# Kernel optimization log

Hardware: AMD Instinct MI355X
Metric: run time of the kernel (lower is better)

## Reference

```python
import jax, jax.numpy as jnp
import numpy as np

B, T, D, F, E, K, L, S = 8, 1024, 512, 1024, 8, 2, 2, 64
SE, SH = 64, 128  # subject_embed_dim, style_hidden_dim


def setup_inputs() -> dict:
    key = jax.random.key(0)
    ks = jax.random.split(key, 16)
    r = lambda i, shape, s=0.05: (jax.random.normal(ks[i], shape, jnp.float32) * s)
    return dict(
        x=jax.random.normal(ks[0], (B, T, D), jnp.float32),
        subject_ids=jax.random.randint(ks[1], (B,), 0, S),
        # per-layer LayerNorm params (L, D)
        ln_g=jnp.ones((L, D), jnp.float32), ln_b=jnp.zeros((L, D), jnp.float32),
        # per-layer SubjectStyleAlignment params (weights stored (in, out))
        subj_emb=r(2, (L, S, SE), 0.02),
        h1_w=r(3, (L, SE, SH)), h1_b=jnp.zeros((L, SH), jnp.float32),
        h2_w=r(4, (L, SH, SH)), h2_b=jnp.zeros((L, SH), jnp.float32),
        s1_w=r(5, (L, SH, SH // 2)), s1_b=jnp.zeros((L, SH // 2), jnp.float32),
        s2_w=r(6, (L, SH // 2, 2 * D)), s2_b=jnp.zeros((L, 2 * D), jnp.float32),
        # shared TopKRouter: Linear(D, D//2) -> ReLU -> Linear(D//2, E)
        g1_w=r(7, (D, D // 2)), g1_b=jnp.zeros((D // 2,), jnp.float32),
        g2_w=r(8, (D // 2, E)), g2_b=jnp.zeros((E,), jnp.float32),
        # shared ExpertPool of GLU experts (no bias)
        wi0=r(9, (E, D, F)), wi1=r(10, (E, D, F)), wo=r(11, (E, F, D)),
    )


def _layernorm(x, g, b):
    m = x.mean(-1, keepdims=True)
    v = x.var(-1, keepdims=True)  # biased, matches torch LayerNorm
    return (x - m) / jnp.sqrt(v + 1e-5) * g + b


def reference(x, subject_ids, ln_g, ln_b, subj_emb, h1_w, h1_b, h2_w, h2_b,
              s1_w, s1_b, s2_w, s2_b, g1_w, g1_b, g2_w, g2_b, wi0, wi1, wo):
    Bs, Ts, Ds = x.shape
    for l in range(L):  # small fixed layer loop; expert pool + router are shared
        res = x
        h = _layernorm(x, ln_g[l], ln_b[l])
        # SubjectStyleAlignment: instance norm over time axis per (B, D) channel
        mu = h.mean(1, keepdims=True)
        var = h.var(1, keepdims=True)
        hn = (h - mu) / jnp.sqrt(var + 1e-8)
        e = subj_emb[l][subject_ids]                               # (B, SE)
        hh = jax.nn.relu(e @ h1_w[l] + h1_b[l]) @ h2_w[l] + h2_b[l]
        sp = jax.nn.relu(hh @ s1_w[l] + s1_b[l]) @ s2_w[l] + s2_b[l]  # (B, 2D)
        gamma = jax.nn.softplus(sp[:, :Ds]) + 1e-8
        beta = sp[:, Ds:]
        h = hn * gamma[:, None, :] + beta[:, None, :]
        # Router (shared across layers)
        hf = h.reshape(-1, Ds)                                     # (N, D)
        logits = jax.nn.relu(hf @ g1_w + g1_b) @ g2_w + g2_b       # (N, E)
        probs = jax.nn.softmax(logits, -1)
        gates, idx = jax.lax.top_k(probs, K)                       # (N, K)
        gates = gates / (gates.sum(-1, keepdims=True) + 1e-8)
        # combine weights: cw[n, e] = sum_k gates[n,k] * [idx[n,k]==e]
        cw = (jax.nn.one_hot(idx, E, dtype=hf.dtype) * gates[..., None]).sum(1)  # (N, E)
        # GLU experts, computed dense over E then gated-combined
        hid = jax.nn.relu(jnp.einsum('nd,edf->enf', hf, wi0)) \
              * jnp.einsum('nd,edf->enf', hf, wi1)                 # (E, N, F)
        eo = jnp.einsum('enf,efd->end', hid, wo)                   # (E, N, D)
        y = jnp.einsum('ne,end->nd', cw, eo)                       # (N, D)
        x = res + y.reshape(Bs, Ts, Ds)
    return x
```

## Files before the change

### kernel.cpp

```cpp
#include <hip/hip_runtime.h>

typedef unsigned short u16;
typedef unsigned int   u32;
typedef _Float16       f16;
typedef __attribute__((ext_vector_type(8))) _Float16 f16x8;
typedef __attribute__((ext_vector_type(4))) float    f32x4;
typedef __attribute__((ext_vector_type(4))) double   dbl4;

#define NSLOT_ 16384

__device__ __forceinline__ u16 f16bits(f16 h){ union{f16 f; u16 u;} x; x.f = h; return x.u; }

__device__ __forceinline__ void gl_lds16(const void* gptr, void* lptr){
  __builtin_amdgcn_global_load_lds((const __attribute__((address_space(1))) u32*)gptr,
                                   (__attribute__((address_space(3))) u32*)lptr, 16, 0, 0);
}

__device__ __forceinline__ int roff(int row, int lks){
  return ((row >> 1) << 6) + ((lks ^ ((row >> 1) & 3)) << 4) + ((row & 1) << 3);
}

__global__ __launch_bounds__(256) void ln_kernel(const float* __restrict__ x,
    const float* __restrict__ g, const float* __restrict__ bb, float* __restrict__ h){
  int n = blockIdx.x, t = threadIdx.x;
  const float* xr = x + ((size_t)n << 9);
  float2 v = *(const float2*)&xr[t*2];
  double vx = v.x, vy = v.y;
  double s = vx + vy;
  double q = vx*vx + vy*vy;
  #pragma unroll
  for (int o = 32; o > 0; o >>= 1){ s += __shfl_down(s, o, 64); q += __shfl_down(q, o, 64); }
  __shared__ double ls[4], lq_[4];
  __shared__ double sm, sv;
  int wid = t >> 6, lane = t & 63;
  if (lane == 0){ ls[wid] = s; lq_[wid] = q; }
  __syncthreads();
  if (t == 0){
    double S = ls[0]+ls[1]+ls[2]+ls[3], Q = lq_[0]+lq_[1]+lq_[2]+lq_[3];
    double mean = S * (1.0/512.0);
    double var  = Q * (1.0/512.0) - mean*mean;
    sm = mean; sv = 1.0/sqrt(var + 1e-5);
  }
  __syncthreads();
  double mean = sm, inv = sv;
  int d = t*2;
  float2 o;
  o.x = (float)((vx - mean)*inv*(double)g[d]   + (double)bb[d]);
  o.y = (float)((vy - mean)*inv*(double)g[d+1] + (double)bb[d+1]);
  *(float2*)&h[((size_t)n<<9) + d] = o;
}

__global__ __launch_bounds__(256) void colstats(const float* __restrict__ h,
    double* __restrict__ cs, double* __restrict__ cq){
  int bid = blockIdx.x;
  int b = bid >> 3, ch = bid & 7;
  int t = threadIdx.x;
  int col = ch*64 + (t & 63);
  int tp = t >> 6;
  const float* base = h + ((size_t)b << 19);
  double s = 0.0, q = 0.0;
  for (int tt = tp; tt < 1024; tt += 4){
    double v = (double)base[((size_t)tt << 9) + col];
    s += v; q += v*v;
  }
  __shared__ double ls[4][64], lq[4][64];
  ls[tp][t & 63] = s; lq[tp][t & 63] = q;
  __syncthreads();
  if (tp == 0){
    double S = ls[0][t]+ls[1][t]+ls[2][t]+ls[3][t];
    double Q = lq[0][t]+lq[1][t]+lq[2][t]+lq[3][t];
    cs[(b<<9)+col] = S; cq[(b<<9)+col] = Q;
  }
}

__global__ __launch_bounds__(256) void subj_kernel(const int* __restrict__ sid,
    const float* __restrict__ semb,
    const float* __restrict__ h1w, const float* __restrict__ h1b,
    const float* __restrict__ h2w, const float* __restrict__ h2b,
    const float* __restrict__ s1w, const float* __restrict__ s1b,
    const float* __restrict__ s2w, const float* __restrict__ s2b,
    const double* __restrict__ cs, const double* __restrict__ cq,
    double* __restrict__ a64, double* __restrict__ c64, int l){
  __shared__ double ev[64], hid1[128], hh[128], sh[64], sp[1024];
  int t = threadIdx.x;
  int b = blockIdx.x;
  int s = sid[b];
  if (t < 64) ev[t] = (double)semb[l*4096 + s*64 + t];
  __syncthreads();
  if (t < 128){
    double acc = (double)h1b[l*128 + t];
    for (int i = 0; i < 64; ++i) acc += ev[i]*(double)h1w[l*8192 + i*128 + t];
    hid1[t] = acc > 0.0 ? acc : 0.0;
  }
  __syncthreads();
  if (t < 128){
    double acc = (double)h2b[l*128 + t];
    for (int i = 0; i < 128; ++i) acc += hid1[i]*(double)h2w[l*16384 + i*128 + t];
    hh[t] = acc;
  }
  __syncthreads();
  if (t < 64){
    double acc = (double)s1b[l*64 + t];
    for (int i = 0; i < 128; ++i) acc += hh[i]*(double)s1w[l*8192 + i*64 + t];
    sh[t] = acc > 0.0 ? acc : 0.0;
  }
  __syncthreads();
  for (int m = t; m < 1024; m += 256){
    double acc = (double)s2b[l*1024 + m];
    for (int j = 0; j < 64; ++j) acc += sh[j]*(double)s2w[l*65536 + j*1024 + m];
    sp[m] = acc;
  }
  __syncthreads();
  for (int d = t; d < 512; d += 256){
    double mu  = cs[(b<<9)+d] * (1.0/1024.0);
    double var = cq[(b<<9)+d] * (1.0/1024.0) - mu*mu;
    double inv = 1.0/sqrt(var + 1e-8);
    double spv = sp[d];
    double gamma = (spv > 30.0 ? spv : log1p(exp(spv))) + 1e-8;
    double beta  = sp[512 + d];
    double A = gamma * inv;
    a64[(b<<9)+d] = A;
    c64[(b<<9)+d] = beta - mu*A;
  }
}

__global__ __launch_bounds__(256) void hfcast(const float* __restrict__ h,
    const double* __restrict__ a64, const double* __restrict__ c64,
    u16* __restrict__ hfh, u16* __restrict__ hfl){
  size_t i0 = ((size_t)blockIdx.x*256 + threadIdx.x) * 8;
  int n = (int)(i0 >> 9);
  int d0 = (int)(i0 & 511);
  int b = n >> 10;
// ... 111 lines not shown
      double v = l0[e];
      if (v > b1){ b2 = b1; i2 = i1; b1 = v; i1 = e; }
      else if (v > b2){ b2 = v; i2 = e; }
    }
    double pr1 = p[i1]/s, pr2 = p[i2]/s;
    double den = pr1 + pr2 + 1e-8;
    int n = tok0 + t;
    idxo[2*n] = i1; idxo[2*n+1] = i2;
    wo_[2*n] = (float)(pr1/den); wo_[2*n+1] = (float)(pr2/den);
    atomicAdd(&lcnt[i1], 1); atomicAdd(&lcnt[i2], 1);
  }
  __syncthreads();
  if (t < 8) atomicAdd(&counts[t], lcnt[t]);
}

__global__ void offsets_kernel(const int* __restrict__ counts, int* __restrict__ offs,
                               int* __restrict__ cur){
  if (threadIdx.x == 0 && blockIdx.x == 0){
    int run = 0;
    for (int e = 0; e < 8; ++e){ offs[e] = run; run += counts[e]; cur[e] = 0; }
  }
}

__global__ __launch_bounds__(256) void scatter_kernel(const int* __restrict__ idx,
    const int* __restrict__ offs, int* __restrict__ cur,
    int* __restrict__ tok_of, int* __restrict__ slot_of){
  __shared__ int lcnt[8], lbase[8];
  int t = threadIdx.x;
  int n = blockIdx.x*256 + t;
  if (t < 8) lcnt[t] = 0;
  __syncthreads();
  int e0 = idx[2*n], e1 = idx[2*n+1];
  int p0 = atomicAdd(&lcnt[e0], 1);
  int p1 = atomicAdd(&lcnt[e1], 1);
  __syncthreads();
  if (t < 8) lbase[t] = atomicAdd(&cur[t], lcnt[t]);
  __syncthreads();
  int s0 = offs[e0] + lbase[e0] + p0;
  int s1 = offs[e1] + lbase[e1] + p1;
  tok_of[s0] = n; tok_of[s1] = n;
  slot_of[2*n] = s0; slot_of[2*n+1] = s1;
}

__global__ __launch_bounds__(256) void cvtT16(const float* __restrict__ src,
    u16* __restrict__ dh, u16* __restrict__ dl, int R, int C){
  int bx = blockIdx.x;
  int tilesC = C >> 5, tilesR = R >> 5;
  int e = bx / (tilesR*tilesC);
  int rem = bx % (tilesR*tilesC);
  int rt = rem / tilesC, ct = rem % tilesC;
  __shared__ float tile[32][33];
  int t = threadIdx.x;
  int j = t & 31, i0 = t >> 5;
  const float* s = src + (size_t)e*R*C + (size_t)(rt*32)*C + ct*32;
  for (int ii = i0; ii < 32; ii += 8) tile[ii][j] = s[(size_t)ii*C + j];
  __syncthreads();
  size_t ob = (size_t)e*R*C + (size_t)(ct*32)*R + rt*32;
  for (int ii = i0; ii < 32; ii += 8){
    float v = tile[j][ii];
    f16 hi = (f16)v;
    float rem2 = (v - (float)hi) * 2048.f;
    f16 lo = (f16)rem2;
    dh[ob + (size_t)ii*R + j] = f16bits(hi);
    dl[ob + (size_t)ii*R + j] = f16bits(lo);
  }
}

__global__ __launch_bounds__(256) void up1_kernel(const u16* __restrict__ hfh,
    const u16* __restrict__ hfl,
    const u16* __restrict__ w0h, const u16* __restrict__ w0l,
    const u16* __restrict__ w1h, const u16* __restrict__ w1l,
    const int* __restrict__ tok_of, const int* __restrict__ offs, const int* __restrict__ counts,
    u16* __restrict__ hidh, u16* __restrict__ hidl){
  int bx = blockIdx.x;
  int e  = bx >> 11;
  int mt = (bx >> 4) & 127;
  int nt = bx & 15;
  int base = offs[e], cnt = counts[e];
  int row0 = mt << 7;
  if (row0 >= cnt) return;
  __shared__ __align__(16) u16 Ah[2][4096], Alo[2][4096];
  __shared__ __align__(16) u16 B0h[2][2048], B0l[2][2048], B1h[2][2048], B1l[2][2048];
  int t = threadIdx.x, w = t >> 6, l = t & 63;
  int wm = w >> 1, wn = w & 1;
  int lr = l & 15, lks = l >> 4;
  int riw = ((l >> 3) << 1) | (l & 1);
  int kc16s = ((((l >> 1) & 3) ^ ((l >> 3) & 3)) << 3);
  int ar1 = w*16 + riw;
  int tokA1, tokA2;
  { int ss = base + row0 + ar1;      ss = ss < NSLOT_ ? ss : NSLOT_-1; tokA1 = tok_of[ss]; }
  { int ss = base + row0 + 64 + ar1; ss = ss < NSLOT_ ? ss : NSLOT_-1; tokA2 = tok_of[ss]; }
  const u16* sAh1 = hfh + ((size_t)tokA1 << 9) + kc16s;
  const u16* sAh2 = hfh + ((size_t)tokA2 << 9) + kc16s;
  const u16* sAl1 = hfl + ((size_t)tokA1 << 9) + kc16s;
  const u16* sAl2 = hfl + ((size_t)tokA2 << 9) + kc16s;
  size_t bcol = (size_t)(e*1024 + nt*64);
  size_t bci = (bcol + (size_t)ar1) << 9;
  const u16* sB0h = w0h + bci + kc16s;
  const u16* sB0l = w0l + bci + kc16s;
  const u16* sB1h = w1h + bci + kc16s;
  const u16* sB1l = w1l + bci + kc16s;
  int aoff[4], boff[2];
  #pragma unroll
  for (int mi = 0; mi < 4; ++mi) aoff[mi] = roff(wm*64 + mi*16 + lr, lks);
  #pragma unroll
  for (int ni = 0; ni < 2; ++ni) boff[ni] = roff(wn*32 + ni*16 + lr, lks);
  f32x4 hh0[4][2], cr0[4][2], hh1[4][2], cr1[4][2];
  #pragma unroll
  for (int i = 0; i < 4; ++i)
    #pragma unroll
    for (int j = 0; j < 2; ++j)
      #pragma unroll
      for (int r = 0; r < 4; ++r){ hh0[i][j][r]=0.f; cr0[i][j][r]=0.f; hh1[i][j][r]=0.f; cr1[i][j][r]=0.f; }
#define STG_U(buf, kc) do{ \
    gl_lds16(sAh1 + (kc), &Ah[buf][t*8]); \
    gl_lds16(sAh2 + (kc), &Ah[buf][2048 + t*8]); \
    gl_lds16(sAl1 + (kc), &Alo[buf][t*8]); \
    gl_lds16(sAl2 + (kc), &Alo[buf][2048 + t*8]); \
    gl_lds16(sB0h + (kc), &B0h[buf][t*8]); \
    gl_lds16(sB0l + (kc), &B0l[buf][t*8]); \
    gl_lds16(sB1h + (kc), &B1h[buf][t*8]); \
    gl_lds16(sB1l + (kc), &B1l[buf][t*8]); }while(0)
  STG_U(0, 0);
  for (int ks = 0; ks < 16; ++ks){
    int cur = ks & 1;
    __syncthreads();
    if (ks < 15) STG_U(cur^1, (ks+1)*32);
    f16x8 ah[4], al[4], b0hv[2], b0lv[2], b1hv[2], b1lv[2];
    #pragma unroll
    for (int mi = 0; mi < 4; ++mi){
      ah[mi] = *(const f16x8*)&Ah[cur][aoff[mi]];
      al[mi] = *(const f16x8*)&Alo[cur][aoff[mi]];
    }
    #pragma unroll
    for (int ni = 0; ni < 2; ++ni){
      b0hv[ni] = *(const f16x8*)&B0h[cur][boff[ni]];
      b0lv[ni] = *(const f16x8*)&B0l[cur][boff[ni]];
      b1hv[ni] = *(const f16x8*)&B1h[cur][boff[ni]];
      b1lv[ni] = *(const f16x8*)&B1l[cur][boff[ni]];
    }
    #pragma unroll
    for (int mi = 0; mi < 4; ++mi)
      #pragma unroll
      for (int ni = 0; ni < 2; ++ni){
        hh0[mi][ni] = __builtin_amdgcn_mfma_f32_16x16x32_f16(ah[mi], b0hv[ni], hh0[mi][ni], 0, 0, 0);
        hh1[mi][ni] = __builtin_amdgcn_mfma_f32_16x16x32_f16(ah[mi], b1hv[ni], hh1[mi][ni], 0, 0, 0);
        cr0[mi][ni] = __builtin_amdgcn_mfma_f32_16x16x32_f16(ah[mi], b0lv[ni], cr0[mi][ni], 0, 0, 0);
        cr0[mi][ni] = __builtin_amdgcn_mfma_f32_16x16x32_f16(al[mi], b0hv[ni], cr0[mi][ni], 0, 0, 0);
        cr1[mi][ni] = __builtin_amdgcn_mfma_f32_16x16x32_f16(ah[mi], b1lv[ni], cr1[mi][ni], 0, 0, 0);
        cr1[mi][ni] = __builtin_amdgcn_mfma_f32_16x16x32_f16(al[mi], b1hv[ni], cr1[mi][ni], 0, 0, 0);
      }
  }
#undef STG_U
  #pragma unroll
  for (int mi = 0; mi < 4; ++mi){
    int rb = row0 + wm*64 + mi*16 + lks*4;
    #pragma unroll
    for (int r = 0; r < 4; ++r){
      int rr = rb + r;
      if (rr < cnt){
        size_t orow = ((size_t)(base + rr) << 10) + nt*64;
        #pragma unroll
        for (int ni = 0; ni < 2; ++ni){
          int col = wn*32 + ni*16 + lr;
          float u0 = hh0[mi][ni][r] + cr0[mi][ni][r]*(1.f/2048.f);
          float u1 = hh1[mi][ni][r] + cr1[mi][ni][r]*(1.f/2048.f);
          u0 = u0 > 0.f ? u0 : 0.f;
          float v = u0*u1;
          f16 vh = (f16)v;
          float rem = (v - (float)vh)*2048.f;
          hidh[orow + col] = f16bits(vh);
          hidl[orow + col] = f16bits((f16)rem);
        }
      }
    }
  }
}

__global__ __launch_bounds__(256) void down1_kernel(const u16* __restrict__ hidh,
    const u16* __restrict__ hidl, const u16* __restrict__ wdh, const u16* __restrict__ wdl,
    const int* __restrict__ offs, const int* __restrict__ counts, float* __restrict__ eo){
  int bx = blockIdx.x;
  int e  = bx >> 10;
  int mt = (bx >> 3) & 127;
  int nt = bx & 7;
  int base = offs[e], cnt = counts[e];
  int row0 = mt << 7;
  if (row0 >= cnt) return;
  __shared__ __align__(16) u16 Ah[2][4096], Alo[2][4096];
  __shared__ __align__(16) u16 Bh[2][2048], Bl[2][2048];
  int t = threadIdx.x, w = t >> 6, l = t & 63;
  int wm = w >> 1, wn = w & 1;
  int lr = l & 15, lks = l >> 4;
  int riw = ((l >> 3) << 1) | (l & 1);
  int kc16s = ((((l >> 1) & 3) ^ ((l >> 3) & 3)) << 3);
  int ar1 = w*16 + riw;
  int sA1c = base + row0 + ar1;      sA1c = sA1c < NSLOT_ ? sA1c : NSLOT_-1;
  int sA2c = base + row0 + 64 + ar1; sA2c = sA2c < NSLOT_ ? sA2c : NSLOT_-1;
  const u16* sAh1 = hidh + ((size_t)sA1c << 10) + kc16s;
  const u16* sAh2 = hidh + ((size_t)sA2c << 10) + kc16s;
  const u16* sAl1 = hidl + ((size_t)sA1c << 10) + kc16s;
  const u16* sAl2 = hidl + ((size_t)sA2c << 10) + kc16s;
  size_t bcol = (size_t)(e*512 + nt*64);
  size_t bci = (bcol + (size_t)ar1) << 10;
  const u16* sBh = wdh + bci + kc16s;
  const u16* sBl = wdl + bci + kc16s;
  int aoff[4], boff[2];
  #pragma unroll
  for (int mi = 0; mi < 4; ++mi) aoff[mi] = roff(wm*64 + mi*16 + lr, lks);
  #pragma unroll
  for (int ni = 0; ni < 2; ++ni) boff[ni] = roff(wn*32 + ni*16 + lr, lks);
  f32x4 hh[4][2], cr[4][2];
  #pragma unroll
  for (int i = 0; i < 4; ++i)
    #pragma unroll
    for (int j = 0; j < 2; ++j)
      #pragma unroll
      for (int r = 0; r < 4; ++r){ hh[i][j][r]=0.f; cr[i][j][r]=0.f; }
#define STG_D(buf, kc) do{ \
    gl_lds16(sAh1 + (kc), &Ah[buf][t*8]); \
    gl_lds16(sAh2 + (kc), &Ah[buf][2048 + t*8]); \
    gl_lds16(sAl1 + (kc), &Alo[buf][t*8]); \
    gl_lds16(sAl2 + (kc), &Alo[buf][2048 + t*8]); \
    gl_lds16(sBh + (kc), &Bh[buf][t*8]); \
    gl_lds16(sBl + (kc), &Bl[buf][t*8]); }while(0)
  STG_D(0, 0);
  for (int ks = 0; ks < 32; ++ks){
    int cur = ks & 1;
    __syncthreads();
    if (ks < 31) STG_D(cur^1, (ks+1)*32);
    f16x8 ah[4], al[4], bh[2], bl[2];
    #pragma unroll
    for (int mi = 0; mi < 4; ++mi){
      ah[mi] = *(const f16x8*)&Ah[cur][aoff[mi]];
      al[mi] = *(const f16x8*)&Alo[cur][aoff[mi]];
    }
    #pragma unroll
    for (int ni = 0; ni < 2; ++ni){
      bh[ni] = *(const f16x8*)&Bh[cur][boff[ni]];
      bl[ni] = *(const f16x8*)&Bl[cur][boff[ni]];
    }
    #pragma unroll
    for (int mi = 0; mi < 4; ++mi)
      #pragma unroll
      for (int ni = 0; ni < 2; ++ni){
        hh[mi][ni] = __builtin_amdgcn_mfma_f32_16x16x32_f16(ah[mi], bh[ni], hh[mi][ni], 0, 0, 0);
        cr[mi][ni] = __builtin_amdgcn_mfma_f32_16x16x32_f16(ah[mi], bl[ni], cr[mi][ni], 0, 0, 0);
        cr[mi][ni] = __builtin_amdgcn_mfma_f32_16x16x32_f16(al[mi], bh[ni], cr[mi][ni], 0, 0, 0);
      }
  }
#undef STG_D
  #pragma unroll
  for (int mi = 0; mi < 4; ++mi){
    int rb = row0 + wm*64 + mi*16 + lks*4;
    #pragma unroll
    for (int r = 0; r < 4; ++r){
      int rr = rb + r;
      if (rr < cnt){
        float* orow = eo + (((size_t)(base + rr)) << 9) + nt*64;
        #pragma unroll
        for (int ni = 0; ni < 2; ++ni)
          orow[wn*32 + ni*16 + lr] = hh[mi][ni][r] + cr[mi][ni][r]*(1.f/2048.f);
      }
    }
  }
}

__global__ __launch_bounds__(256) void uph_kernel(const u16* __restrict__ hfh,
    const u16* __restrict__ w0h, const u16* __restrict__ w1h,
    const int* __restrict__ tok_of, const int* __restrict__ offs, const int* __restrict__ counts,
    u16* __restrict__ hidh){
  int bx = blockIdx.x;
  int e  = bx >> 11;
  int mt = (bx >> 4) & 127;
  int nt = bx & 15;
  int base = offs[e], cnt = counts[e];
  int row0 = mt << 7;
  if (row0 >= cnt) return;
  __shared__ __align__(16) u16 Ah[2][4096];
  __shared__ __align__(16) u16 B0h[2][2048], B1h[2][2048];
  int t = threadIdx.x, w = t >> 6, l = t & 63;
  int wm = w >> 1, wn = w & 1;
  int lr = l & 15, lks = l >> 4;
  int riw = ((l >> 3) << 1) | (l & 1);
  int kc16s = ((((l >> 1) & 3) ^ ((l >> 3) & 3)) << 3);
  int ar1 = w*16 + riw;
  int tokA1, tokA2;
  { int ss = base + row0 + ar1;      ss = ss < NSLOT_ ? ss : NSLOT_-1; tokA1 = tok_of[ss]; }
  { int ss = base + row0 + 64 + ar1; ss = ss < NSLOT_ ? ss : NSLOT_-1; tokA2 = tok_of[ss]; }
  const u16* sAh1 = hfh + ((size_t)tokA1 << 9) + kc16s;
  const u16* sAh2 = hfh + ((size_t)tokA2 << 9) + kc16s;
  size_t bcol = (size_t)(e*1024 + nt*64);
  size_t bci = (bcol + (size_t)ar1) << 9;
  const u16* sB0 = w0h + bci + kc16s;
  const u16* sB1 = w1h + bci + kc16s;
  int aoff[4], boff[2];
  #pragma unroll
  for (int mi = 0; mi < 4; ++mi) aoff[mi] = roff(wm*64 + mi*16 + lr, lks);
  #pragma unroll
  for (int ni = 0; ni < 2; ++ni) boff[ni] = roff(wn*32 + ni*16 + lr, lks);
  f32x4 hh0[4][2], hh1[4][2];
  #pragma unroll
  for (int i = 0; i < 4; ++i)
    #pragma unroll
    for (int j = 0; j < 2; ++j)
      #pragma unroll
      for (int r = 0; r < 4; ++r){ hh0[i][j][r]=0.f; hh1[i][j][r]=0.f; }
#define STG_UH(buf, kc) do{ \
    gl_lds16(sAh1 + (kc), &Ah[buf][t*8]); \
    gl_lds16(sAh2 + (kc), &Ah[buf][2048 + t*8]); \
    gl_lds16(sB0 + (kc), &B0h[buf][t*8]); \
    gl_lds16(sB1 + (kc), &B1h[buf][t*8]); }while(0)
  STG_UH(0, 0);
  for (int ks = 0; ks < 16; ++ks){
    int cur = ks & 1;
    __syncthreads();
    if (ks < 15) STG_UH(cur^1, (ks+1)*32);
    f16x8 ah[4], b0v[2], b1v[2];
    #pragma unroll
    for (int mi = 0; mi < 4; ++mi) ah[mi] = *(const f16x8*)&Ah[cur][aoff[mi]];
    #pragma unroll
    for (int ni = 0; ni < 2; ++ni){
      b0v[ni] = *(const f16x8*)&B0h[cur][boff[ni]];
      b1v[ni] = *(const f16x8*)&B1h[cur][boff[ni]];
    }
    #pragma unroll
    for (int mi = 0; mi < 4; ++mi)
      #pragma unroll
      for (int ni = 0; ni < 2; ++ni){
        hh0[mi][ni] = __builtin_amdgcn_mfma_f32_16x16x32_f16(ah[mi], b0v[ni], hh0[mi][ni], 0, 0, 0);
        hh1[mi][ni] = __builtin_amdgcn_mfma_f32_16x16x32_f16(ah[mi], b1v[ni], hh1[mi][ni], 0, 0, 0);
      }
  }
#undef STG_UH
  #pragma unroll
  for (int mi = 0; mi < 4; ++mi){
    int rb = row0 + wm*64 + mi*16 + lks*4;
    #pragma unroll
    for (int r = 0; r < 4; ++r){
      int rr = rb + r;
      if (rr < cnt){
        size_t orow = ((size_t)(base + rr) << 10) + nt*64;
        #pragma unroll
        for (int ni = 0; ni < 2; ++ni){
          int col = wn*32 + ni*16 + lr;
          float u0 = hh0[mi][ni][r];
          u0 = u0 > 0.f ? u0 : 0.f;
          hidh[orow + col] = f16bits((f16)(u0*hh1[mi][ni][r]));
        }
      }
    }
  }
}

__global__ __launch_bounds__(256) void dnh_kernel(const u16* __restrict__ hidh,
    const u16* __restrict__ wdh,
    const int* __restrict__ offs, const int* __restrict__ counts, float* __restrict__ eo){
  int bx = blockIdx.x;
  int e  = bx >> 10;
  int mt = (bx >> 3) & 127;
  int nt = bx & 7;
  int base = offs[e], cnt = counts[e];
  int row0 = mt << 7;
  if (row0 >= cnt) return;
  __shared__ __align__(16) u16 Ah[2][4096];
  __shared__ __align__(16) u16 Bh[2][2048];
  int t = threadIdx.x, w = t >> 6, l = t & 63;
  int wm = w >> 1, wn = w & 1;
  int lr = l & 15, lks = l >> 4;
  int riw = ((l >> 3) << 1) | (l & 1);
  int kc16s = ((((l >> 1) & 3) ^ ((l >> 3) & 3)) << 3);
  int ar1 = w*16 + riw;
  int sA1c = base + row0 + ar1;      sA1c = sA1c < NSLOT_ ? sA1c : NSLOT_-1;
  int sA2c = base + row0 + 64 + ar1; sA2c = sA2c < NSLOT_ ? sA2c : NSLOT_-1;
  const u16* sAh1 = hidh + ((size_t)sA1c << 10) + kc16s;
  const u16* sAh2 = hidh + ((size_t)sA2c << 10) + kc16s;
  size_t bcol = (size_t)(e*512 + nt*64);
  const u16* sB = wdh + ((bcol + (size_t)ar1) << 10) + kc16s;
  int aoff[4], boff[2];
  #pragma unroll
  for (int mi = 0; mi < 4; ++mi) aoff[mi] = roff(wm*64 + mi*16 + lr, lks);
  #pragma unroll
  for (int ni = 0; ni < 2; ++ni) boff[ni] = roff(wn*32 + ni*16 + lr, lks);
  f32x4 hh[4][2];
  #pragma unroll
  for (int i = 0; i < 4; ++i)
    #pragma unroll
    for (int j = 0; j < 2; ++j)
      #pragma unroll
      for (int r = 0; r < 4; ++r) hh[i][j][r] = 0.f;
#define STG_DH(buf, kc) do{ \
    gl_lds16(sAh1 + (kc), &Ah[buf][t*8]); \
    gl_lds16(sAh2 + (kc), &Ah[buf][2048 + t*8]); \
    gl_lds16(sB + (kc), &Bh[buf][t*8]); }while(0)
  STG_DH(0, 0);
  for (int ks = 0; ks < 32; ++ks){
    int cur = ks & 1;
    __syncthreads();
    if (ks < 31) STG_DH(cur^1, (ks+1)*32);
    f16x8 ah[4], bh[2];
    #pragma unroll
    for (int mi = 0; mi < 4; ++mi) ah[mi] = *(const f16x8*)&Ah[cur][aoff[mi]];
    #pragma unroll
    for (int ni = 0; ni < 2; ++ni) bh[ni] = *(const f16x8*)&Bh[cur][boff[ni]];
    #pragma unroll
    for (int mi = 0; mi < 4; ++mi)
      #pragma unroll
      for (int ni = 0; ni < 2; ++ni)
        hh[mi][ni] = __builtin_amdgcn_mfma_f32_16x16x32_f16(ah[mi], bh[ni], hh[mi][ni], 0, 0, 0);
  }
#undef STG_DH
  #pragma unroll
  for (int mi = 0; mi < 4; ++mi){
    int rb = row0 + wm*64 + mi*16 + lks*4;
    #pragma unroll
    for (int r = 0; r < 4; ++r){
      int rr = rb + r;
      if (rr < cnt){
        float* orow = eo + (((size_t)(base + rr)) << 9) + nt*64;
        #pragma unroll
        for (int ni = 0; ni < 2; ++ni)
          orow[wn*32 + ni*16 + lr] = hh[mi][ni][r];
      }
    }
  }
}

__global__ __launch_bounds__(128) void gather_kernel(const float* __restrict__ xin,
    const float* __restrict__ eo, const int* __restrict__ slot_of, const float* __restrict__ wv,
    float* __restrict__ out){
  int n = blockIdx.x, t = threadIdx.x;
  int s0 = slot_of[2*n], s1 = slot_of[2*n+1];
  double w0 = wv[2*n], w1 = wv[2*n+1];
  float4 xi = *(const float4*)&xin[((size_t)n << 9) + t*4];
  float4 e0 = *(const float4*)&eo[((size_t)s0 << 9) + t*4];
  float4 e1 = *(const float4*)&eo[((size_t)s1 << 9) + t*4];
  float4 o;
  o.x = (float)((double)xi.x + w0*(double)e0.x + w1*(double)e1.x);
  o.y = (float)((double)xi.y + w0*(double)e0.y + w1*(double)e1.y);
  o.z = (float)((double)xi.z + w0*(double)e0.z + w1*(double)e1.z);
  o.w = (float)((double)xi.w + w0*(double)e0.w + w1*(double)e1.w);
  *(float4*)&out[((size_t)n << 9) + t*4] = o;
}

extern "C" void kernel_launch(void* const* d_in, const int* in_sizes, int n_in,
                              void* d_out, int out_size, void* d_ws, size_t ws_size,
                              hipStream_t stream) {
  (void)in_sizes; (void)n_in; (void)out_size; (void)ws_size;
  const float* x0   = (const float*)d_in[0];
  const int*   sid  = (const int*)  d_in[1];
  const float* ln_g = (const float*)d_in[2];
  const float* ln_b = (const float*)d_in[3];
  const float* semb = (const float*)d_in[4];
  const float* h1w  = (const float*)d_in[5];
  const float* h1b  = (const float*)d_in[6];
  const float* h2w  = (const float*)d_in[7];
  const float* h2b  = (const float*)d_in[8];
  const float* s1w  = (const float*)d_in[9];
  const float* s1b  = (const float*)d_in[10];
  const float* s2w  = (const float*)d_in[11];
  const float* s2b  = (const float*)d_in[12];
  const float* g1w  = (const float*)d_in[13];
  const float* g1b  = (const float*)d_in[14];
  const float* g2w  = (const float*)d_in[15];
  const float* g2b  = (const float*)d_in[16];
  const float* wi0  = (const float*)d_in[17];
  const float* wi1  = (const float*)d_in[18];
  const float* wo   = (const float*)d_in[19];

  char* W = (char*)d_ws;
  float*  h      = (float*)(W + 0);
  u16*    hfh    = (u16*)  (W + 16777216ULL);
  u16*    hfl    = (u16*)  (W + 25165824ULL);
  float*  eo32   = (float*)(W + 0);
  u16*    hid16h = (u16*)  (W + 33554432ULL);
  u16*    hid16l = (u16*)  (W + 67108864ULL);
  u16*    w0Th   = (u16*)  (W + 100663296ULL);
  u16*    w0Tl   = (u16*)  (W + 109051904ULL);
  u16*    w1Th   = (u16*)  (W + 117440512ULL);
  u16*    w1Tl   = (u16*)  (W + 125829120ULL);
  u16*    woTh   = (u16*)  (W + 134217728ULL);
  u16*    woTl   = (u16*)  (W + 142606336ULL);
  u16*    g1Th   = (u16*)  (W + 150994944ULL);
  u16*    g1Tl   = (u16*)  (W + 151257088ULL);
  double* cs     = (double*)(W + 151519232ULL);
  double* cq     = (double*)(W + 151552000ULL);
  double* a64    = (double*)(W + 151584768ULL);
  double* c64    = (double*)(W + 151617536ULL);
  int*    idxa   = (int*)   (W + 151650304ULL);
  float*  warr   = (float*) (W + 151715840ULL);
  int*    tok_of = (int*)   (W + 151781376ULL);
  int*    slot_of= (int*)   (W + 151846912ULL);
  int*    counts = (int*)   (W + 151912448ULL);
  int*    cur    = counts + 8;
  int*    offs   = counts + 16;

  cvtT16<<<4096, 256, 0, stream>>>(wi0, w0Th, w0Tl, 512, 1024);
  cvtT16<<<4096, 256, 0, stream>>>(wi1, w1Th, w1Tl, 512, 1024);
  cvtT16<<<4096, 256, 0, stream>>>(wo,  woTh, woTl, 1024, 512);
  cvtT16<<<128,  256, 0, stream>>>(g1w, g1Th, g1Tl, 512, 256);

  for (int l = 0; l < 2; ++l){
    const float* xin = l ? (const float*)d_out : x0;
    ln_kernel<<<8192, 256, 0, stream>>>(xin, ln_g + l*512, ln_b + l*512, h);
    colstats<<<64, 256, 0, stream>>>(h, cs, cq);
    subj_kernel<<<8, 256, 0, stream>>>(sid, semb, h1w, h1b, h2w, h2b, s1w, s1b, s2w, s2b,
                                       cs, cq, a64, c64, l);
    hfcast<<<2048, 256, 0, stream>>>(h, a64, c64, hfh, hfl);
    zero_counts<<<1, 64, 0, stream>>>(counts);
    gate2_kernel<<<512, 256, 0, stream>>>(hfh, hfl, g1Th, g1Tl, g1b, g2w, g2b, idxa, warr, counts);
    offsets_kernel<<<1, 1, 0, stream>>>(counts, offs, cur);
    scatter_kernel<<<32, 256, 0, stream>>>(idxa, offs, cur, tok_of, slot_of);
    if (l == 0){
      up1_kernel<<<16384, 256, 0, stream>>>(hfh, hfl, w0Th, w0Tl, w1Th, w1Tl,
                                            tok_of, offs, counts, hid16h, hid16l);
      down1_kernel<<<8192, 256, 0, stream>>>(hid16h, hid16l, woTh, woTl, offs, counts, eo32);
    } else {
      uph_kernel<<<16384, 256, 0, stream>>>(hfh, w0Th, w1Th, tok_of, offs, counts, hid16h);
      dnh_kernel<<<8192, 256, 0, stream>>>(hid16h, woTh, offs, counts, eo32);
    }
    gather_kernel<<<8192, 128, 0, stream>>>(xin, eo32, slot_of, warr, (float*)d_out);
  }
}
```

Before: 868.7 us.

## Widen MoE GEMM N-tiles and fuse layer-0 gather with layer-1 LayerNorm

The down and up expert GEMM kernels (dnh, uph, down1) now use 128-column output tiles instead of 64, halving the grid and reusing each staged A tile across twice as many outputs. up1 keeps 64 columns but switches its warp layout from 2x2 to 4x1 over rows. The layer loop is unrolled, and a new gather_ln kernel fuses the layer-0 residual combine with the layer-1 LayerNorm, which removes one full pass over the activations. eo32 moves to its own workspace region so it no longer overlaps h. The wider tiles raise accumulator register and LDS use, which can lower occupancy.

```diff
diff --git a/kernel.cpp b/kernel.cpp
--- a/kernel.cpp
+++ b/kernel.cpp
@@ -48,6 +48,49 @@
   o.x = (float)((vx - mean)*inv*(double)g[d]   + (double)bb[d]);
   o.y = (float)((vy - mean)*inv*(double)g[d+1] + (double)bb[d+1]);
   *(float2*)&h[((size_t)n<<9) + d] = o;
+}
+
+__global__ __launch_bounds__(128) void gather_ln(const float* __restrict__ xin,
+    const float* __restrict__ eo, const int* __restrict__ slot_of, const float* __restrict__ wv,
+    const float* __restrict__ g, const float* __restrict__ bb,
+    float* __restrict__ out, float* __restrict__ h){
+  int n = blockIdx.x, t = threadIdx.x;
+  int s0 = slot_of[2*n], s1 = slot_of[2*n+1];
+  double w0 = wv[2*n], w1 = wv[2*n+1];
+  float4 xi = *(const float4*)&xin[((size_t)n << 9) + t*4];
+  float4 e0 = *(const float4*)&eo[((size_t)s0 << 9) + t*4];
+  float4 e1 = *(const float4*)&eo[((size_t)s1 << 9) + t*4];
+  double o0 = (double)xi.x + w0*(double)e0.x + w1*(double)e1.x;
+  double o1 = (double)xi.y + w0*(double)e0.y + w1*(double)e1.y;
+  double o2 = (double)xi.z + w0*(double)e0.z + w1*(double)e1.z;
+  double o3 = (double)xi.w + w0*(double)e0.w + w1*(double)e1.w;
+  float4 o; o.x = (float)o0; o.y = (float)o1; o.z = (float)o2; o.w = (float)o3;
+  *(float4*)&out[((size_t)n << 9) + t*4] = o;
+  double vx = o.x, vy = o.y, vz = o.z, vw = o.w;
+  double s = vx+vy+vz+vw;
+  double q = vx*vx+vy*vy+vz*vz+vw*vw;
+  #pragma unroll
+  for (int off = 32; off > 0; off >>= 1){ s += __shfl_down(s, off, 64); q += __shfl_down(q, off, 64); }
+  __shared__ double ls[2], lq_[2];
+  __shared__ double sm, sv;
+  int wid = t >> 6, lane = t & 63;
+  if (lane == 0){ ls[wid] = s; lq_[wid] = q; }
+  __syncthreads();
+  if (t == 0){
+    double S = ls[0]+ls[1], Q = lq_[0]+lq_[1];
+    double mean = S * (1.0/512.0);
+    double var  = Q * (1.0/512.0) - mean*mean;
+    sm = mean; sv = 1.0/sqrt(var + 1e-5);
+  }
+  __syncthreads();
+  double mean = sm, inv = sv;
+  int d = t*4;
+  float4 ho;
+  ho.x = (float)((vx - mean)*inv*(double)g[d]   + (double)bb[d]);
+  ho.y = (float)((vy - mean)*inv*(double)g[d+1] + (double)bb[d+1]);
+  ho.z = (float)((vz - mean)*inv*(double)g[d+2] + (double)bb[d+2]);
+  ho.w = (float)((vw - mean)*inv*(double)g[d+3] + (double)bb[d+3]);
+  *(float4*)&h[((size_t)n<<9) + d] = ho;
 }
 
 __global__ __launch_bounds__(256) void colstats(const float* __restrict__ h,
@@ -325,7 +368,6 @@
   __shared__ __align__(16) u16 Ah[2][4096], Alo[2][4096];
   __shared__ __align__(16) u16 B0h[2][2048], B0l[2][2048], B1h[2][2048], B1l[2][2048];
   int t = threadIdx.x, w = t >> 6, l = t & 63;
-  int wm = w >> 1, wn = w & 1;
   int lr = l & 15, lks = l >> 4;
   int riw = ((l >> 3) << 1) | (l & 1);
   int kc16s = ((((l >> 1) & 3) ^ ((l >> 3) & 3)) << 3);
@@ -343,16 +385,16 @@
   const u16* sB0l = w0l + bci + kc16s;
   const u16* sB1h = w1h + bci + kc16s;
   const u16* sB1l = w1l + bci + kc16s;
-  int aoff[4], boff[2];
-  #pragma unroll
-  for (int mi = 0; mi < 4; ++mi) aoff[mi] = roff(wm*64 + mi*16 + lr, lks);
-  #pragma unroll
-  for (int ni = 0; ni < 2; ++ni) boff[ni] = roff(wn*32 + ni*16 + lr, lks);
-  f32x4 hh0[4][2], cr0[4][2], hh1[4][2], cr1[4][2];
-  #pragma unroll
-  for (int i = 0; i < 4; ++i)
-    #pragma unroll
-    for (int j = 0; j < 2; ++j)
+  int aoff[2], boff[4];
+  #pragma unroll
+  for (int mi = 0; mi < 2; ++mi) aoff[mi] = roff(w*32 + mi*16 + lr, lks);
+  #pragma unroll
+  for (int ni = 0; ni < 4; ++ni) boff[ni] = roff(ni*16 + lr, lks);
+  f32x4 hh0[2][4], cr0[2][4], hh1[2][4], cr1[2][4];
+  #pragma unroll
+  for (int i = 0; i < 2; ++i)
+    #pragma unroll
+    for (int j = 0; j < 4; ++j)
       #pragma unroll
       for (int r = 0; r < 4; ++r){ hh0[i][j][r]=0.f; cr0[i][j][r]=0.f; hh1[i][j][r]=0.f; cr1[i][j][r]=0.f; }
 #define STG_U(buf, kc) do{ \
@@ -369,23 +411,23 @@
     int cur = ks & 1;
     __syncthreads();
     if (ks < 15) STG_U(cur^1, (ks+1)*32);
-    f16x8 ah[4], al[4], b0hv[2], b0lv[2], b1hv[2], b1lv[2];
-    #pragma unroll
-    for (int mi = 0; mi < 4; ++mi){
+    f16x8 ah[2], al[2], b0hv[4], b0lv[4], b1hv[4], b1lv[4];
+    #pragma unroll
+    for (int mi = 0; mi < 2; ++mi){
       ah[mi] = *(const f16x8*)&Ah[cur][aoff[mi]];
       al[mi] = *(const f16x8*)&Alo[cur][aoff[mi]];
     }
     #pragma unroll
-    for (int ni = 0; ni < 2; ++ni){
+    for (int ni = 0; ni < 4; ++ni){
       b0hv[ni] = *(const f16x8*)&B0h[cur][boff[ni]];
       b0lv[ni] = *(const f16x8*)&B0l[cur][boff[ni]];
       b1hv[ni] = *(const f16x8*)&B1h[cur][boff[ni]];
       b1lv[ni] = *(const f16x8*)&B1l[cur][boff[ni]];
     }
     #pragma unroll
-    for (int mi = 0; mi < 4; ++mi)
+    for (int mi = 0; mi < 2; ++mi)
       #pragma unroll
-      for (int ni = 0; ni < 2; ++ni){
+      for (int ni = 0; ni < 4; ++ni){
         hh0[mi][ni] = __builtin_amdgcn_mfma_f32_16x16x32_f16(ah[mi], b0hv[ni], hh0[mi][ni], 0, 0, 0);
         hh1[mi][ni] = __builtin_amdgcn_mfma_f32_16x16x32_f16(ah[mi], b1hv[ni], hh1[mi][ni], 0, 0, 0);
         cr0[mi][ni] = __builtin_amdgcn_mfma_f32_16x16x32_f16(ah[mi], b0lv[ni], cr0[mi][ni], 0, 0, 0);
@@ -396,16 +438,16 @@
   }
 #undef STG_U
   #pragma unroll
-  for (int mi = 0; mi < 4; ++mi){
-    int rb = row0 + wm*64 + mi*16 + lks*4;
+  for (int mi = 0; mi < 2; ++mi){
+    int rb = row0 + w*32 + mi*16 + lks*4;
     #pragma unroll
     for (int r = 0; r < 4; ++r){
       int rr = rb + r;
       if (rr < cnt){
         size_t orow = ((size_t)(base + rr) << 10) + nt*64;
         #pragma unroll
-        for (int ni = 0; ni < 2; ++ni){
-          int col = wn*32 + ni*16 + lr;
+        for (int ni = 0; ni < 4; ++ni){
+          int col = ni*16 + lr;
           float u0 = hh0[mi][ni][r] + cr0[mi][ni][r]*(1.f/2048.f);
           float u1 = hh1[mi][ni][r] + cr1[mi][ni][r]*(1.f/2048.f);
           u0 = u0 > 0.f ? u0 : 0.f;
@@ -424,14 +466,14 @@
     const u16* __restrict__ hidl, const u16* __restrict__ wdh, const u16* __restrict__ wdl,
     const int* __restrict__ offs, const int* __restrict__ counts, float* __restrict__ eo){
   int bx = blockIdx.x;
-  int e  = bx >> 10;
-  int mt = (bx >> 3) & 127;
-  int nt = bx & 7;
+  int e  = bx >> 9;
+  int mt = (bx >> 2) & 127;
+  int nt = bx & 3;
   int base = offs[e], cnt = counts[e];
   int row0 = mt << 7;
   if (row0 >= cnt) return;
   __shared__ __align__(16) u16 Ah[2][4096], Alo[2][4096];
-  __shared__ __align__(16) u16 Bh[2][2048], Bl[2][2048];
+  __shared__ __align__(16) u16 Bh[2][4096], Bl[2][4096];
   int t = threadIdx.x, w = t >> 6, l = t & 63;
   int wm = w >> 1, wn = w & 1;
   int lr = l & 15, lks = l >> 4;
@@ -444,20 +486,21 @@
   const u16* sAh2 = hidh + ((size_t)sA2c << 10) + kc16s;
   const u16* sAl1 = hidl + ((size_t)sA1c << 10) + kc16s;
   const u16* sAl2 = hidl + ((size_t)sA2c << 10) + kc16s;
-  size_t bcol = (size_t)(e*512 + nt*64);
-  size_t bci = (bcol + (size_t)ar1) << 10;
-  const u16* sBh = wdh + bci + kc16s;
-  const u16* sBl = wdl + bci + kc16s;
-  int aoff[4], boff[2];
+  size_t bcol = (size_t)(e*512 + nt*128);
+  const u16* sBh1 = wdh + ((bcol + (size_t)ar1) << 10) + kc16s;
+  const u16* sBh2 = wdh + ((bcol + 64 + (size_t)ar1) << 10) + kc16s;
+  const u16* sBl1 = wdl + ((bcol + (size_t)ar1) << 10) + kc16s;
+  const u16* sBl2 = wdl + ((bcol + 64 + (size_t)ar1) << 10) + kc16s;
+  int aoff[4], boff[4];
   #pragma unroll
   for (int mi = 0; mi < 4; ++mi) aoff[mi] = roff(wm*64 + mi*16 + lr, lks);
   #pragma unroll
-  for (int ni = 0; ni < 2; ++ni) boff[ni] = roff(wn*32 + ni*16 + lr, lks);
-  f32x4 hh[4][2], cr[4][2];
+  for (int ni = 0; ni < 4; ++ni) boff[ni] = roff(wn*64 + ni*16 + lr, lks);
+  f32x4 hh[4][4], cr[4][4];
   #pragma unroll
   for (int i = 0; i < 4; ++i)
     #pragma unroll
-    for (int j = 0; j < 2; ++j)
+    for (int j = 0; j < 4; ++j)
       #pragma unroll
       for (int r = 0; r < 4; ++r){ hh[i][j][r]=0.f; cr[i][j][r]=0.f; }
 #define STG_D(buf, kc) do{ \
@@ -465,28 +508,30 @@
     gl_lds16(sAh2 + (kc), &Ah[buf][2048 + t*8]); \
     gl_lds16(sAl1 + (kc), &Alo[buf][t*8]); \
     gl_lds16(sAl2 + (kc), &Alo[buf][2048 + t*8]); \
-    gl_lds16(sBh + (kc), &Bh[buf][t*8]); \
-    gl_lds16(sBl + (kc), &Bl[buf][t*8]); }while(0)
+    gl_lds16(sBh1 + (kc), &Bh[buf][t*8]); \
+    gl_lds16(sBh2 + (kc), &Bh[buf][2048 + t*8]); \
+    gl_lds16(sBl1 + (kc), &Bl[buf][t*8]); \
+    gl_lds16(sBl2 + (kc), &Bl[buf][2048 + t*8]); }while(0)
   STG_D(0, 0);
   for (int ks = 0; ks < 32; ++ks){
     int cur = ks & 1;
     __syncthreads();
     if (ks < 31) STG_D(cur^1, (ks+1)*32);
-    f16x8 ah[4], al[4], bh[2], bl[2];
+    f16x8 ah[4], al[4], bh[4], bl[4];
     #pragma unroll
     for (int mi = 0; mi < 4; ++mi){
       ah[mi] = *(const f16x8*)&Ah[cur][aoff[mi]];
       al[mi] = *(const f16x8*)&Alo[cur][aoff[mi]];
     }
     #pragma unroll
-    for (int ni = 0; ni < 2; ++ni){
+    for (int ni = 0; ni < 4; ++ni){
       bh[ni] = *(const f16x8*)&Bh[cur][boff[ni]];
       bl[ni] = *(const f16x8*)&Bl[cur][boff[ni]];
     }
     #pragma unroll
     for (int mi = 0; mi < 4; ++mi)
       #pragma unroll
-      for (int ni = 0; ni < 2; ++ni){
+      for (int ni = 0; ni < 4; ++ni){
         hh[mi][ni] = __builtin_amdgcn_mfma_f32_16x16x32_f16(ah[mi], bh[ni], hh[mi][ni], 0, 0, 0);
         cr[mi][ni] = __builtin_amdgcn_mfma_f32_16x16x32_f16(ah[mi], bl[ni], cr[mi][ni], 0, 0, 0);
         cr[mi][ni] = __builtin_amdgcn_mfma_f32_16x16x32_f16(al[mi], bh[ni], cr[mi][ni], 0, 0, 0);
@@ -500,10 +545,10 @@
     for (int r = 0; r < 4; ++r){
       int rr = rb + r;
       if (rr < cnt){
-        float* orow = eo + (((size_t)(base + rr)) << 9) + nt*64;
+        float* orow = eo + (((size_t)(base + rr)) << 9) + nt*128;
         #pragma unroll
-        for (int ni = 0; ni < 2; ++ni)
-          orow[wn*32 + ni*16 + lr] = hh[mi][ni][r] + cr[mi][ni][r]*(1.f/2048.f);
+        for (int ni = 0; ni < 4; ++ni)
+          orow[wn*64 + ni*16 + lr] = hh[mi][ni][r] + cr[mi][ni][r]*(1.f/2048.f);
       }
     }
   }
@@ -514,14 +559,14 @@
     const int* __restrict__ tok_of, const int* __restrict__ offs, const int* __restrict__ counts,
     u16* __restrict__ hidh){
   int bx = blockIdx.x;
-  int e  = bx >> 11;
-  int mt = (bx >> 4) & 127;
-  int nt = bx & 15;
+  int e  = bx >> 10;
+  int mt = (bx >> 3) & 127;
+  int nt = bx & 7;
   int base = offs[e], cnt = counts[e];
   int row0 = mt << 7;
   if (row0 >= cnt) return;
   __shared__ __align__(16) u16 Ah[2][4096];
-  __shared__ __align__(16) u16 B0h[2][2048], B1h[2][2048];
+  __shared__ __align__(16) u16 B0[2][4096], B1[2][4096];
   int t = threadIdx.x, w = t >> 6, l = t & 63;
   int wm = w >> 1, wn = w & 1;
   int lr = l & 15, lks = l >> 4;
@@ -533,44 +578,47 @@
   { int ss = base + row0 + 64 + ar1; ss = ss < NSLOT_ ? ss : NSLOT_-1; tokA2 = tok_of[ss]; }
   const u16* sAh1 = hfh + ((size_t)tokA1 << 9) + kc16s;
   const u16* sAh2 = hfh + ((size_t)tokA2 << 9) + kc16s;
-  size_t bcol = (size_t)(e*1024 + nt*64);
-  size_t bci = (bcol + (size_t)ar1) << 9;
-  const u16* sB0 = w0h + bci + kc16s;
-  const u16* sB1 = w1h + bci + kc16s;
-  int aoff[4], boff[2];
+  size_t bcol = (size_t)(e*1024 + nt*128);
+  const u16* sB0a = w0h + ((bcol + (size_t)ar1) << 9) + kc16s;
+  const u16* sB0b = w0h + ((bcol + 64 + (size_t)ar1) << 9) + kc16s;
+  const u16* sB1a = w1h + ((bcol + (size_t)ar1) << 9) + kc16s;
+  const u16* sB1b = w1h + ((bcol + 64 + (size_t)ar1) << 9) + kc16s;
+  int aoff[4], boff[4];
   #pragma unroll
   for (int mi = 0; mi < 4; ++mi) aoff[mi] = roff(wm*64 + mi*16 + lr, lks);
   #pragma unroll
-  for (int ni = 0; ni < 2; ++ni) boff[ni] = roff(wn*32 + ni*16 + lr, lks);
-  f32x4 hh0[4][2], hh1[4][2];
+  for (int ni = 0; ni < 4; ++ni) boff[ni] = roff(wn*64 + ni*16 + lr, lks);
+  f32x4 hh0[4][4], hh1[4][4];
   #pragma unroll
   for (int i = 0; i < 4; ++i)
     #pragma unroll
-    for (int j = 0; j < 2; ++j)
+    for (int j = 0; j < 4; ++j)
       #pragma unroll
       for (int r = 0; r < 4; ++r){ hh0[i][j][r]=0.f; hh1[i][j][r]=0.f; }
 #define STG_UH(buf, kc) do{ \
     gl_lds16(sAh1 + (kc), &Ah[buf][t*8]); \
     gl_lds16(sAh2 + (kc), &Ah[buf][2048 + t*8]); \
-    gl_lds16(sB0 + (kc), &B0h[buf][t*8]); \
-    gl_lds16(sB1 + (kc), &B1h[buf][t*8]); }while(0)
+    gl_lds16(sB0a + (kc), &B0[buf][t*8]); \
+    gl_lds16(sB0b + (kc), &B0[buf][2048 + t*8]); \
+    gl_lds16(sB1a + (kc), &B1[buf][t*8]); \
+    gl_lds16(sB1b + (kc), &B1[buf][2048 + t*8]); }while(0)
   STG_UH(0, 0);
   for (int ks = 0; ks < 16; ++ks){
     int cur = ks & 1;
     __syncthreads();
     if (ks < 15) STG_UH(cur^1, (ks+1)*32);
-    f16x8 ah[4], b0v[2], b1v[2];
+    f16x8 ah[4], b0v[4], b1v[4];
     #pragma unroll
     for (int mi = 0; mi < 4; ++mi) ah[mi] = *(const f16x8*)&Ah[cur][aoff[mi]];
     #pragma unroll
-    for (int ni = 0; ni < 2; ++ni){
-      b0v[ni] = *(const f16x8*)&B0h[cur][boff[ni]];
-      b1v[ni] = *(const f16x8*)&B1h[cur][boff[ni]];
+    for (int ni = 0; ni < 4; ++ni){
+      b0v[ni] = *(const f16x8*)&B0[cur][boff[ni]];
+      b1v[ni] = *(const f16x8*)&B1[cur][boff[ni]];
     }
     #pragma unroll
     for (int mi = 0; mi < 4; ++mi)
       #pragma unroll
-      for (int ni = 0; ni < 2; ++ni){
+      for (int ni = 0; ni < 4; ++ni){
         hh0[mi][ni] = __builtin_amdgcn_mfma_f32_16x16x32_f16(ah[mi], b0v[ni], hh0[mi][ni], 0, 0, 0);
         hh1[mi][ni] = __builtin_amdgcn_mfma_f32_16x16x32_f16(ah[mi], b1v[ni], hh1[mi][ni], 0, 0, 0);
       }
@@ -583,10 +631,10 @@
     for (int r = 0; r < 4; ++r){
       int rr = rb + r;
       if (rr < cnt){
-        size_t orow = ((size_t)(base + rr) << 10) + nt*64;
+        size_t orow = ((size_t)(base + rr) << 10) + nt*128;
         #pragma unroll
-        for (int ni = 0; ni < 2; ++ni){
-          int col = wn*32 + ni*16 + lr;
+        for (int ni = 0; ni < 4; ++ni){
+          int col = wn*64 + ni*16 + lr;
           float u0 = hh0[mi][ni][r];
           u0 = u0 > 0.f ? u0 : 0.f;
           hidh[orow + col] = f16bits((f16)(u0*hh1[mi][ni][r]));
@@ -600,14 +648,14 @@
     const u16* __restrict__ wdh,
     const int* __restrict__ offs, const int* __restrict__ counts, float* __restrict__ eo){
   int bx = blockIdx.x;
-  int e  = bx >> 10;
-  int mt = (bx >> 3) & 127;
-  int nt = bx & 7;
+  int e  = bx >> 9;
+  int mt = (bx >> 2) & 127;
+  int nt = bx & 3;
   int base = offs[e], cnt = counts[e];
   int row0 = mt << 7;
   if (row0 >= cnt) return;
   __shared__ __align__(16) u16 Ah[2][4096];
-  __shared__ __align__(16) u16 Bh[2][2048];
+  __shared__ __align__(16) u16 Bh[2][4096];
   int t = threadIdx.x, w = t >> 6, l = t & 63;
   int wm = w >> 1, wn = w & 1;
   int lr = l & 15, lks = l >> 4;
@@ -618,38 +666,40 @@
   int sA2c = base + row0 + 64 + ar1; sA2c = sA2c < NSLOT_ ? sA2c : NSLOT_-1;
   const u16* sAh1 = hidh + ((size_t)sA1c << 10) + kc16s;
   const u16* sAh2 = hidh + ((size_t)sA2c << 10) + kc16s;
-  size_t bcol = (size_t)(e*512 + nt*64);
-  const u16* sB = wdh + ((bcol + (size_t)ar1) << 10) + kc16s;
-  int aoff[4], boff[2];
+  size_t bcol = (size_t)(e*512 + nt*128);
+  const u16* sB1 = wdh + ((bcol + (size_t)ar1) << 10) + kc16s;
+  const u16* sB2 = wdh + ((bcol + 64 + (size_t)ar1) << 10) + kc16s;
+  int aoff[4], boff[4];
   #pragma unroll
   for (int mi = 0; mi < 4; ++mi) aoff[mi] = roff(wm*64 + mi*16 + lr, lks);
   #pragma unroll
-  for (int ni = 0; ni < 2; ++ni) boff[ni] = roff(wn*32 + ni*16 + lr, lks);
-  f32x4 hh[4][2];
+  for (int ni = 0; ni < 4; ++ni) boff[ni] = roff(wn*64 + ni*16 + lr, lks);
+  f32x4 hh[4][4];
   #pragma unroll
   for (int i = 0; i < 4; ++i)
     #pragma unroll
-    for (int j = 0; j < 2; ++j)
+    for (int j = 0; j < 4; ++j)
       #pragma unroll
       for (int r = 0; r < 4; ++r) hh[i][j][r] = 0.f;
 #define STG_DH(buf, kc) do{ \
     gl_lds16(sAh1 + (kc), &Ah[buf][t*8]); \
     gl_lds16(sAh2 + (kc), &Ah[buf][2048 + t*8]); \
-    gl_lds16(sB + (kc), &Bh[buf][t*8]); }while(0)
+    gl_lds16(sB1 + (kc), &Bh[buf][t*8]); \
+    gl_lds16(sB2 + (kc), &Bh[buf][2048 + t*8]); }while(0)
   STG_DH(0, 0);
   for (int ks = 0; ks < 32; ++ks){
     int cur = ks & 1;
     __syncthreads();
     if (ks < 31) STG_DH(cur^1, (ks+1)*32);
-    f16x8 ah[4], bh[2];
+    f16x8 ah[4], bh[4];
     #pragma unroll
     for (int mi = 0; mi < 4; ++mi) ah[mi] = *(const f16x8*)&Ah[cur][aoff[mi]];
     #pragma unroll
-    for (int ni = 0; ni < 2; ++ni) bh[ni] = *(const f16x8*)&Bh[cur][boff[ni]];
+    for (int ni = 0; ni < 4; ++ni) bh[ni] = *(const f16x8*)&Bh[cur][boff[ni]];
     #pragma unroll
     for (int mi = 0; mi < 4; ++mi)
       #pragma unroll
-      for (int ni = 0; ni < 2; ++ni)
+      for (int ni = 0; ni < 4; ++ni)
         hh[mi][ni] = __builtin_amdgcn_mfma_f32_16x16x32_f16(ah[mi], bh[ni], hh[mi][ni], 0, 0, 0);
   }
 #undef STG_DH
@@ -660,10 +710,10 @@
     for (int r = 0; r < 4; ++r){
       int rr = rb + r;
       if (rr < cnt){
-        float* orow = eo + (((size_t)(base + rr)) << 9) + nt*64;
+        float* orow = eo + (((size_t)(base + rr)) << 9) + nt*128;
         #pragma unroll
-        for (int ni = 0; ni < 2; ++ni)
-          orow[wn*32 + ni*16 + lr] = hh[mi][ni][r];
+        for (int ni = 0; ni < 4; ++ni)
+          orow[wn*64 + ni*16 + lr] = hh[mi][ni][r];
       }
     }
   }
@@ -715,7 +765,7 @@
   float*  h      = (float*)(W + 0);
   u16*    hfh    = (u16*)  (W + 16777216ULL);
   u16*    hfl    = (u16*)  (W + 25165824ULL);
-  float*  eo32   = (float*)(W + 0);
+  float*  eo32   = (float*)(W + 167772160ULL);
   u16*    hid16h = (u16*)  (W + 33554432ULL);
   u16*    hid16l = (u16*)  (W + 67108864ULL);
   u16*    w0Th   = (u16*)  (W + 100663296ULL);
@@ -743,25 +793,29 @@
   cvtT16<<<4096, 256, 0, stream>>>(wo,  woTh, woTl, 1024, 512);
   cvtT16<<<128,  256, 0, stream>>>(g1w, g1Th, g1Tl, 512, 256);
 
-  for (int l = 0; l < 2; ++l){
-    const float* xin = l ? (const float*)d_out : x0;
-    ln_kernel<<<8192, 256, 0, stream>>>(xin, ln_g + l*512, ln_b + l*512, h);
-    colstats<<<64, 256, 0, stream>>>(h, cs, cq);
-    subj_kernel<<<8, 256, 0, stream>>>(sid, semb, h1w, h1b, h2w, h2b, s1w, s1b, s2w, s2b,
-                                       cs, cq, a64, c64, l);
-    hfcast<<<2048, 256, 0, stream>>>(h, a64, c64, hfh, hfl);
-    zero_counts<<<1, 64, 0, stream>>>(counts);
-    gate2_kernel<<<512, 256, 0, stream>>>(hfh, hfl, g1Th, g1Tl, g1b, g2w, g2b, idxa, warr, counts);
-    offsets_kernel<<<1, 1, 0, stream>>>(counts, offs, cur);
-    scatter_kernel<<<32, 256, 0, stream>>>(idxa, offs, cur, tok_of, slot_of);
-    if (l == 0){
-      up1_kernel<<<16384, 256, 0, stream>>>(hfh, hfl, w0Th, w0Tl, w1Th, w1Tl,
-                                            tok_of, offs, counts, hid16h, hid16l);
-      down1_kernel<<<8192, 256, 0, stream>>>(hid16h, hid16l, woTh, woTl, offs, counts, eo32);
-    } else {
-      uph_kernel<<<16384, 256, 0, stream>>>(hfh, w0Th, w1Th, tok_of, offs, counts, hid16h);
-      dnh_kernel<<<8192, 256, 0, stream>>>(hid16h, woTh, offs, counts, eo32);
-    }
-    gather_kernel<<<8192, 128, 0, stream>>>(xin, eo32, slot_of, warr, (float*)d_out);
-  }
-}
+  ln_kernel<<<8192, 256, 0, stream>>>(x0, ln_g, ln_b, h);
+  colstats<<<64, 256, 0, stream>>>(h, cs, cq);
+  subj_kernel<<<8, 256, 0, stream>>>(sid, semb, h1w, h1b, h2w, h2b, s1w, s1b, s2w, s2b,
+                                     cs, cq, a64, c64, 0);
+  hfcast<<<2048, 256, 0, stream>>>(h, a64, c64, hfh, hfl);
+  zero_counts<<<1, 64, 0, stream>>>(counts);
+  gate2_kernel<<<512, 256, 0, stream>>>(hfh, hfl, g1Th, g1Tl, g1b, g2w, g2b, idxa, warr, counts);
+  offsets_kernel<<<1, 1, 0, stream>>>(counts, offs, cur);
+  scatter_kernel<<<32, 256, 0, stream>>>(idxa, offs, cur, tok_of, slot_of);
+  up1_kernel<<<16384, 256, 0, stream>>>(hfh, hfl, w0Th, w0Tl, w1Th, w1Tl,
+                                        tok_of, offs, counts, hid16h, hid16l);
+  down1_kernel<<<4096, 256, 0, stream>>>(hid16h, hid16l, woTh, woTl, offs, counts, eo32);
+  gather_ln<<<8192, 128, 0, stream>>>(x0, eo32, slot_of, warr, ln_g + 512, ln_b + 512,
+                                      (float*)d_out, h);
+  colstats<<<64, 256, 0, stream>>>(h, cs, cq);
+  subj_kernel<<<8, 256, 0, stream>>>(sid, semb, h1w, h1b, h2w, h2b, s1w, s1b, s2w, s2b,
+                                     cs, cq, a64, c64, 1);
+  hfcast<<<2048, 256, 0, stream>>>(h, a64, c64, hfh, hfl);
+  zero_counts<<<1, 64, 0, stream>>>(counts);
+  gate2_kernel<<<512, 256, 0, stream>>>(hfh, hfl, g1Th, g1Tl, g1b, g2w, g2b, idxa, warr, counts);
+  offsets_kernel<<<1, 1, 0, stream>>>(counts, offs, cur);
+  scatter_kernel<<<32, 256, 0, stream>>>(idxa, offs, cur, tok_of, slot_of);
+  uph_kernel<<<8192, 256, 0, stream>>>(hfh, w0Th, w1Th, tok_of, offs, counts, hid16h);
+  dnh_kernel<<<4096, 256, 0, stream>>>(hid16h, woTh, offs, counts, eo32);
+  gather_kernel<<<8192, 128, 0, stream>>>((const float*)d_out, eo32, slot_of, warr, (float*)d_out);
+}
```

Result: slower. 1.056 ms (+21.5%).
